# Optimization experiments

Measured on AMD Instinct MI355X. Metric: run time of the kernel, lower is better.

## Reference

```python
import jax, jax.numpy as jnp
import numpy as np

NUM_GROUPS = 32
EPS = 1e-5


def group_norm(x, scale, bias):
    # x: [B, C, L], normalize per (group, batch) over (C//G, L)
    B, C, L = x.shape
    G = NUM_GROUPS
    xg = x.reshape(B, G, C // G, L)
    mean = xg.mean(axis=(2, 3), keepdims=True)
    var = xg.var(axis=(2, 3), keepdims=True)
    xg = (xg - mean) * jax.lax.rsqrt(var + EPS)
    h = xg.reshape(B, C, L)
    return h * scale[None, :, None] + bias[None, :, None]


def setup_inputs() -> dict:
    key = jax.random.key(0)
    ks = jax.random.split(key, 8)
    B, C, L = 8, 512, 2048
    s = 1.0 / np.sqrt(C)
    return {
        "x": jax.random.normal(ks[0], (B, C, L), jnp.float32),
        "gn_scale": jnp.ones((C,), jnp.float32),
        "gn_bias": jnp.zeros((C,), jnp.float32),
        "wq": jax.random.normal(ks[1], (C, C), jnp.float32) * s,
        "bq": jnp.zeros((C,), jnp.float32),
        "wk": jax.random.normal(ks[2], (C, C), jnp.float32) * s,
        "bk": jnp.zeros((C,), jnp.float32),
        "wv": jax.random.normal(ks[3], (C, C), jnp.float32) * s,
        "bv": jnp.zeros((C,), jnp.float32),
        "wo": jax.random.normal(ks[4], (C, C), jnp.float32) * s,
        "bo": jnp.zeros((C,), jnp.float32),
    }


def reference(x, gn_scale, gn_bias, wq, bq, wk, bk, wv, bv, wo, bo):
    B, C, L = x.shape
    h = group_norm(x, gn_scale, gn_bias)  # [B, C, L]
    # 1x1 conv == per-position linear; produce [B, L, C] directly
    q = jnp.einsum('oc,bcl->blo', wq, h) + bq
    k = jnp.einsum('oc,bcl->blo', wk, h) + bk
    v = jnp.einsum('oc,bcl->blo', wv, h) + bv
    scale = jnp.asarray(C, x.dtype) ** -0.5
    w = jnp.einsum('bqc,bkc->bqk', q, k) * scale  # [B, L, L]
    w = jax.nn.softmax(w, axis=-1)
    a = jnp.einsum('bqk,bkc->bqc', w, v)  # [B, L, C]
    out = jnp.einsum('oc,blc->bol', wo, a) + bo[None, :, None]  # [B, C, L]
    return x + out
```

## Files before the change

kernel.cpp:

```cpp
#include <hip/hip_runtime.h>

typedef __attribute__((ext_vector_type(8))) _Float16 half8;
typedef __attribute__((ext_vector_type(4))) float floatx4;

#define AS1 __attribute__((address_space(1)))
#define AS3 __attribute__((address_space(3)))

__device__ __forceinline__ void async_load16(const void* g, void* l) {
  __builtin_amdgcn_global_load_lds((AS1 void*)(unsigned long long)g,
                                   (AS3 void*)(unsigned long long)l, 16, 0, 0);
}

__global__ __launch_bounds__(256) void gn_stats(const float* __restrict__ x,
                                                float* __restrict__ stats) {
  const int bg = blockIdx.x;
  const float4* p4 = (const float4*)(x + (long long)bg * 32768);
  const int t = threadIdx.x;
  float s = 0.f, ss = 0.f;
  for (int i = t; i < 8192; i += 256) {
    float4 v = p4[i];
    s += v.x + v.y + v.z + v.w;
    ss += v.x * v.x + v.y * v.y + v.z * v.z + v.w * v.w;
  }
#pragma unroll
  for (int off = 32; off; off >>= 1) { s += __shfl_down(s, off); ss += __shfl_down(ss, off); }
  __shared__ float rs[4], rss[4];
  if ((t & 63) == 0) { rs[t >> 6] = s; rss[t >> 6] = ss; }
  __syncthreads();
  if (t == 0) {
    s = rs[0] + rs[1] + rs[2] + rs[3];
    ss = rss[0] + rss[1] + rss[2] + rss[3];
    float mean = s * (1.f / 32768.f);
    float var = ss * (1.f / 32768.f) - mean * mean;
    stats[bg] = mean;
    stats[256 + bg] = rsqrtf(var + 1e-5f);
  }
}

__global__ __launch_bounds__(256) void gn_apply(const float* __restrict__ x,
                                                const float* __restrict__ stats,
                                                const float* __restrict__ gsc,
                                                const float* __restrict__ gbi,
                                                _Float16* __restrict__ ht) {
  __shared__ float tile[64][65];
  const int b = blockIdx.z, c0 = blockIdx.y * 64, l0 = blockIdx.x * 64;
  const int t = threadIdx.x, tr = t >> 6, tc = t & 63;
  const float* xb = x + ((long long)b * 512 + c0) * 2048 + l0;
#pragma unroll
  for (int p = 0; p < 16; ++p) {
    int row = tr + p * 4;
    tile[row][tc] = xb[(long long)row * 2048 + tc];
  }
  __syncthreads();
  const int c = c0 + tc;
  const int bg = b * 32 + (c >> 4);
  const float mean = stats[bg], rstd = stats[256 + bg];
  const float sc = gsc[c] * rstd;
  const float off = gbi[c] - mean * sc;
  _Float16* hb = ht + ((long long)b * 2048 + l0) * 512 + c0;
#pragma unroll
  for (int p = 0; p < 16; ++p) {
    int l = tr + p * 4;
    hb[(long long)l * 512 + tc] = (_Float16)(tile[tc][l] * sc + off);
  }
}

__global__ __launch_bounds__(256) void cast_w(const float* __restrict__ w0, const float* __restrict__ w1,
                                              const float* __restrict__ w2, const float* __restrict__ w3,
                                              const float* __restrict__ bq, const float* __restrict__ bk,
                                              _Float16* __restrict__ outw, float* __restrict__ bqk) {
  const long long i = (long long)blockIdx.x * 256 + threadIdx.x;
  if (blockIdx.x < 4096) {
    const int m = (int)(i >> 18);
    const int r = (int)(i & 262143);
    const float* w = (m == 0) ? w0 : (m == 1) ? w1 : (m == 2) ? w2 : w3;
    outw[i] = (_Float16)w[r];
  } else {
    const int j = (int)(i - 4096LL * 256);
    bqk[j] = (j < 512) ? bq[j] : bk[j - 512];
  }
}

template <int BIAS_MODE , int OUT_TYPE , bool RESIDUAL>
__global__ __launch_bounds__(256) void gemm_bt(
    const _Float16* __restrict__ A, long long sA, int lda,
    const _Float16* __restrict__ Bt, long long sB, int ldb,
    void* __restrict__ Cv, long long sC, int ldc,
    const float* __restrict__ bias,
    const float* __restrict__ resid, long long sR,
    float alpha, int K) {
  __shared__ __align__(16) _Float16 lsa[128 * 64];
  __shared__ __align__(16) _Float16 lsb[128 * 64];
  const int tid = threadIdx.x;
  const int wave = tid >> 6, lane = tid & 63;
  const int bz = blockIdx.x;
  const int m0 = blockIdx.y * 128, n0 = blockIdx.z * 128;
  A += (long long)bz * sA;
  Bt += (long long)bz * sB;

  const bool isA = (wave < 2);
  const _Float16* gsrc = isA ? A : Bt;
  const int ld = isA ? lda : ldb;
  const int rbase = (wave & 1) * 64;
  const int t0 = isA ? m0 : n0;
  _Float16* lbase = (isA ? lsa : lsb) + rbase * 64;
  const int grow = t0 + rbase + (lane >> 3);
  const int gcol = ((lane & 7) ^ ((lane >> 3) & 7)) * 8;

  floatx4 acc[4][4] = {};
  const int mw = (wave >> 1) * 64, nw = (wave & 1) * 64;
  const int fm = lane & 15;
  const int quad = lane >> 4;

  for (int k0 = 0; k0 < K; k0 += 64) {
    __syncthreads();
    const _Float16* g = gsrc + (long long)grow * ld + k0 + gcol;
#pragma unroll
    for (int s = 0; s < 8; ++s)
      async_load16(g + (long long)s * 8 * ld, lbase + s * 512);
    __syncthreads();
#pragma unroll
    for (int kk = 0; kk < 2; ++kk) {
      const int ca = quad + 4 * kk;
      const int cs = (ca ^ (fm & 7)) * 8;
      half8 af[4], bfr[4];
#pragma unroll
      for (int i = 0; i < 4; ++i) af[i] = *(const half8*)&lsa[(mw + 16 * i + fm) * 64 + cs];
#pragma unroll
      for (int j = 0; j < 4; ++j) bfr[j] = *(const half8*)&lsb[(nw + 16 * j + fm) * 64 + cs];
#pragma unroll
      for (int i = 0; i < 4; ++i)
#pragma unroll
        for (int j = 0; j < 4; ++j)
          acc[i][j] = __builtin_amdgcn_mfma_f32_16x16x32_f16(af[i], bfr[j], acc[i][j], 0, 0, 0);
    }
  }

  const int r0 = m0 + mw + quad * 4;
  const int c0 = n0 + nw + fm;
#pragma unroll
  for (int i = 0; i < 4; ++i) {
#pragma unroll
    for (int j = 0; j < 4; ++j) {
      const int cc = c0 + 16 * j;
#pragma unroll
      for (int t = 0; t < 4; ++t) {
        const int rr = r0 + 16 * i + t;
        float v = acc[i][j][t] * alpha;
        if (BIAS_MODE == 1) v += bias[cc];
        if (BIAS_MODE == 2) v += bias[rr];
        if (RESIDUAL) v += resid[(long long)bz * sR + (long long)rr * ldc + cc];
        const long long off = (long long)bz * sC + (long long)rr * ldc + cc;
        if (OUT_TYPE == 0) ((float*)Cv)[off] = v;
        else ((_Float16*)Cv)[off] = (_Float16)v;
      }
    }
  }
}

__global__ __launch_bounds__(256) void softmax_inplace(_Float16* __restrict__ S) {
  const long long row = (long long)blockIdx.y * 2048 + blockIdx.x;
  _Float16* p = S + row * 2048;
  const int t = threadIdx.x;
  union U { float4 f; _Float16 h[8]; } u;
  u.f = ((const float4*)p)[t];
  float v[8];
  float mx = -3e38f;
#pragma unroll
  for (int i = 0; i < 8; ++i) { v[i] = (float)u.h[i]; mx = fmaxf(mx, v[i]); }
#pragma unroll
  for (int off = 32; off; off >>= 1) mx = fmaxf(mx, __shfl_down(mx, off));
  __shared__ float red[4];
  if ((t & 63) == 0) red[t >> 6] = mx;
  __syncthreads();
  mx = fmaxf(fmaxf(red[0], red[1]), fmaxf(red[2], red[3]));
  float s = 0.f;
#pragma unroll
  for (int i = 0; i < 8; ++i) { v[i] = __expf(v[i] - mx); s += v[i]; }
#pragma unroll
  for (int off = 32; off; off >>= 1) s += __shfl_down(s, off);
  __syncthreads();
  if ((t & 63) == 0) red[t >> 6] = s;
  __syncthreads();
  s = red[0] + red[1] + red[2] + red[3];
  const float inv = 1.f / s;
#pragma unroll
  for (int i = 0; i < 8; ++i) u.h[i] = (_Float16)(v[i] * inv);
  ((float4*)p)[t] = u.f;
}

extern "C" void kernel_launch(void* const* d_in, const int* in_sizes, int n_in,
                              void* d_out, int out_size, void* d_ws, size_t ws_size,
                              hipStream_t stream) {
  const float* x = (const float*)d_in[0];
  const float* gsc = (const float*)d_in[1];
  const float* gbi = (const float*)d_in[2];
  const float* wq = (const float*)d_in[3];
  const float* bq = (const float*)d_in[4];
  const float* wk = (const float*)d_in[5];
  const float* bk = (const float*)d_in[6];
  const float* wv = (const float*)d_in[7];
  const float* bv = (const float*)d_in[8];
  const float* wo = (const float*)d_in[9];
  const float* bo = (const float*)d_in[10];
  float* out = (float*)d_out;

  char* ws = (char*)d_ws;
  float* stats = (float*)ws;
  float* bqk = (float*)(ws + 2048);
  _Float16* wbf = (_Float16*)(ws + 8192);
  _Float16* ht = wbf + 4 * 262144;
  const long long EB = 8LL * 2048 * 512;
  _Float16* qk = ht + EB;
  _Float16* vm = qk + 2 * EB;
  _Float16* Sb = vm + EB;
  _Float16* at = ht;

  gn_stats<<<256, 256, 0, stream>>>(x, stats);
  gn_apply<<<dim3(32, 8, 8), 256, 0, stream>>>(x, stats, gsc, gbi, ht);
  cast_w<<<4100, 256, 0, stream>>>(wq, wk, wv, wo, bq, bk, wbf, bqk);

  const float scale = 0.044194173824159216f;
  gemm_bt<1, 1, false><<<dim3(8, 16, 8), 256, 0, stream>>>(
      ht, 1048576LL, 512, wbf, 0LL, 512, qk, 2097152LL, 1024, bqk, nullptr, 0LL, 1.f, 512);
  gemm_bt<2, 1, false><<<dim3(8, 4, 16), 256, 0, stream>>>(
      wbf + 2 * 262144, 0LL, 512, ht, 1048576LL, 512, vm, 1048576LL, 2048, bv, nullptr, 0LL, 1.f, 512);
  gemm_bt<0, 1, false><<<dim3(8, 16, 16), 256, 0, stream>>>(
      qk, 2097152LL, 1024, qk + 512, 2097152LL, 1024, Sb, 4194304LL, 2048, nullptr, nullptr, 0LL, scale, 512);
  softmax_inplace<<<dim3(2048, 8), 256, 0, stream>>>(Sb);
  gemm_bt<0, 1, false><<<dim3(8, 16, 4), 256, 0, stream>>>(
      Sb, 4194304LL, 2048, vm, 1048576LL, 2048, at, 1048576LL, 512, nullptr, nullptr, 0LL, 1.f, 2048);
  gemm_bt<2, 0, true><<<dim3(8, 4, 16), 256, 0, stream>>>(
      wbf + 3 * 262144, 0LL, 512, at, 1048576LL, 512, out, 1048576LL, 2048, bo, x, 1048576LL, 1.f, 512);
}
```

Measured before the change: 301.9 us.

## Fuse QK^T, softmax and PV into a single flash-attention kernel

Removes the separate score GEMM, in-place softmax and PV GEMM, and replaces them with one kernel. It keeps the Q fragments in registers, streams 32-key K/V tiles through double-buffered LDS with async global-to-LDS loads, and applies an online softmax with running max and sum. This avoids writing and re-reading the 8x2048x2048 fp16 score matrix and cuts two launches. In exchange it runs at one wave per SIMD with very high register use, and each block re-reads the whole K/V for its batch, which adds L2 pressure.

Measured after the change: 393.9 us. 30.5% more time.

```diff
diff --git a/kernel.cpp b/kernel.cpp
--- a/kernel.cpp
+++ b/kernel.cpp
@@ -158,35 +158,135 @@
   }
 }
 
-__global__ __launch_bounds__(256) void softmax_inplace(_Float16* __restrict__ S) {
-  const long long row = (long long)blockIdx.y * 2048 + blockIdx.x;
-  _Float16* p = S + row * 2048;
-  const int t = threadIdx.x;
-  union U { float4 f; _Float16 h[8]; } u;
-  u.f = ((const float4*)p)[t];
-  float v[8];
-  float mx = -3e38f;
-#pragma unroll
-  for (int i = 0; i < 8; ++i) { v[i] = (float)u.h[i]; mx = fmaxf(mx, v[i]); }
-#pragma unroll
-  for (int off = 32; off; off >>= 1) mx = fmaxf(mx, __shfl_down(mx, off));
-  __shared__ float red[4];
-  if ((t & 63) == 0) red[t >> 6] = mx;
+__global__ __launch_bounds__(256, 1) void flash_attn(
+    const _Float16* __restrict__ qk,
+    const _Float16* __restrict__ vm,
+    _Float16* __restrict__ at) {
+  __shared__ __align__(16) _Float16 kbuf[2][32 * 512];
+  __shared__ __align__(16) _Float16 vbuf[2][512 * 32];
+  __shared__ __align__(16) _Float16 Pls[4][16 * 40];
+  const int tid = threadIdx.x, wave = tid >> 6, lane = tid & 63;
+  const int fm = lane & 15, quad = lane >> 4;
+  const int b = blockIdx.x, q0 = blockIdx.y * 64;
+  const _Float16* qb = qk + (long long)b * 2097152;
+  const _Float16* kb = qb + 512;
+  const _Float16* vb = vm + (long long)b * 1048576;
+
+  half8 qf[16];
+  {
+    const _Float16* qrow = qb + (long long)(q0 + 16 * wave + fm) * 1024 + quad * 8;
+#pragma unroll
+    for (int ks = 0; ks < 16; ++ks) {
+      half8 h = *(const half8*)(qrow + ks * 32);
+#pragma unroll
+      for (int e = 0; e < 8; ++e) h[e] = (_Float16)((float)h[e] * 0.044194173824159216f);
+      qf[ks] = h;
+    }
+  }
+
+  floatx4 o[32] = {};
+  float m_i[4], l_i[4];
+#pragma unroll
+  for (int t = 0; t < 4; ++t) { m_i[t] = -1e30f; l_i[t] = 0.f; }
+
+#pragma unroll
+  for (int s = 0; s < 8; ++s) {
+    int i = s * 256 + tid;
+    int row = i >> 6, ch = i & 63;
+    async_load16(kb + (long long)row * 1024 + ((ch ^ (row & 7)) << 3), &kbuf[0][i * 8]);
+  }
+#pragma unroll
+  for (int s = 0; s < 8; ++s) {
+    int i = s * 256 + tid;
+    int row = i >> 2, ch = i & 3;
+    async_load16(vb + (long long)row * 2048 + ((ch ^ (row & 3)) << 3), &vbuf[0][i * 8]);
+  }
   __syncthreads();
-  mx = fmaxf(fmaxf(red[0], red[1]), fmaxf(red[2], red[3]));
-  float s = 0.f;
-#pragma unroll
-  for (int i = 0; i < 8; ++i) { v[i] = __expf(v[i] - mx); s += v[i]; }
-#pragma unroll
-  for (int off = 32; off; off >>= 1) s += __shfl_down(s, off);
-  __syncthreads();
-  if ((t & 63) == 0) red[t >> 6] = s;
-  __syncthreads();
-  s = red[0] + red[1] + red[2] + red[3];
-  const float inv = 1.f / s;
-#pragma unroll
-  for (int i = 0; i < 8; ++i) u.h[i] = (_Float16)(v[i] * inv);
-  ((float4*)p)[t] = u.f;
+
+  for (int kt = 0; kt < 64; ++kt) {
+    const int cur = kt & 1;
+    if (kt < 63) {
+      const int l0 = (kt + 1) * 32;
+      const int nxt = cur ^ 1;
+#pragma unroll
+      for (int s = 0; s < 8; ++s) {
+        int i = s * 256 + tid;
+        int row = i >> 6, ch = i & 63;
+        async_load16(kb + (long long)(l0 + row) * 1024 + ((ch ^ (row & 7)) << 3),
+                     &kbuf[nxt][i * 8]);
+      }
+#pragma unroll
+      for (int s = 0; s < 8; ++s) {
+        int i = s * 256 + tid;
+        int row = i >> 2, ch = i & 3;
+        async_load16(vb + (long long)row * 2048 + l0 + ((ch ^ (row & 3)) << 3),
+                     &vbuf[nxt][i * 8]);
+      }
+    }
+
+    floatx4 sacc[2] = {};
+#pragma unroll
+    for (int ks = 0; ks < 16; ++ks) {
+#pragma unroll
+      for (int j = 0; j < 2; ++j) {
+        const int ch = (ks * 4 + quad) ^ (fm & 7);
+        half8 bf = *(const half8*)&kbuf[cur][(16 * j + fm) * 512 + ch * 8];
+        sacc[j] = __builtin_amdgcn_mfma_f32_16x16x32_f16(qf[ks], bf, sacc[j], 0, 0, 0);
+      }
+    }
+
+    float alpha[4];
+#pragma unroll
+    for (int t = 0; t < 4; ++t) {
+      float mx = fmaxf(sacc[0][t], sacc[1][t]);
+#pragma unroll
+      for (int d = 1; d < 16; d <<= 1) mx = fmaxf(mx, __shfl_xor(mx, d));
+      float mn = fmaxf(m_i[t], mx);
+      alpha[t] = __expf(m_i[t] - mn);
+      m_i[t] = mn;
+      float rs = 0.f;
+#pragma unroll
+      for (int j = 0; j < 2; ++j) {
+        float p = __expf(sacc[j][t] - mn);
+        sacc[j][t] = p;
+        rs += p;
+      }
+#pragma unroll
+      for (int d = 1; d < 16; d <<= 1) rs += __shfl_xor(rs, d);
+      l_i[t] = l_i[t] * alpha[t] + rs;
+    }
+
+#pragma unroll
+    for (int j = 0; j < 2; ++j)
+#pragma unroll
+      for (int t = 0; t < 4; ++t)
+        Pls[wave][(quad * 4 + t) * 40 + 16 * j + fm] = (_Float16)sacc[j][t];
+
+#pragma unroll
+    for (int j = 0; j < 32; ++j) {
+      o[j][0] *= alpha[0]; o[j][1] *= alpha[1];
+      o[j][2] *= alpha[2]; o[j][3] *= alpha[3];
+    }
+
+    half8 pf = *(const half8*)&Pls[wave][fm * 40 + quad * 8];
+#pragma unroll
+    for (int j = 0; j < 32; ++j) {
+      const int ch = quad ^ (fm & 3);
+      half8 vf = *(const half8*)&vbuf[cur][(16 * j + fm) * 32 + ch * 8];
+      o[j] = __builtin_amdgcn_mfma_f32_16x16x32_f16(pf, vf, o[j], 0, 0, 0);
+    }
+    __syncthreads();
+  }
+
+  float inv[4];
+#pragma unroll
+  for (int t = 0; t < 4; ++t) inv[t] = 1.f / l_i[t];
+  _Float16* ob = at + ((long long)b * 2048 + q0 + 16 * wave) * 512;
+#pragma unroll
+  for (int j = 0; j < 32; ++j)
+#pragma unroll
+    for (int t = 0; t < 4; ++t)
+      ob[(quad * 4 + t) * 512 + 16 * j + fm] = (_Float16)(o[j][t] * inv[t]);
 }
 
 extern "C" void kernel_launch(void* const* d_in, const int* in_sizes, int n_in,
@@ -211,25 +311,19 @@
   _Float16* wbf = (_Float16*)(ws + 8192);
   _Float16* ht = wbf + 4 * 262144;
   const long long EB = 8LL * 2048 * 512;
-  _Float16* qk = ht + EB;
-  _Float16* vm = qk + 2 * EB;
-  _Float16* Sb = vm + EB;
+  _Float16* qkb = ht + EB;
+  _Float16* vm = qkb + 2 * EB;
   _Float16* at = ht;
 
   gn_stats<<<256, 256, 0, stream>>>(x, stats);
   gn_apply<<<dim3(32, 8, 8), 256, 0, stream>>>(x, stats, gsc, gbi, ht);
   cast_w<<<4100, 256, 0, stream>>>(wq, wk, wv, wo, bq, bk, wbf, bqk);
 
-  const float scale = 0.044194173824159216f;
   gemm_bt<1, 1, false><<<dim3(8, 16, 8), 256, 0, stream>>>(
-      ht, 1048576LL, 512, wbf, 0LL, 512, qk, 2097152LL, 1024, bqk, nullptr, 0LL, 1.f, 512);
+      ht, 1048576LL, 512, wbf, 0LL, 512, qkb, 2097152LL, 1024, bqk, nullptr, 0LL, 1.f, 512);
   gemm_bt<2, 1, false><<<dim3(8, 4, 16), 256, 0, stream>>>(
       wbf + 2 * 262144, 0LL, 512, ht, 1048576LL, 512, vm, 1048576LL, 2048, bv, nullptr, 0LL, 1.f, 512);
-  gemm_bt<0, 1, false><<<dim3(8, 16, 16), 256, 0, stream>>>(
-      qk, 2097152LL, 1024, qk + 512, 2097152LL, 1024, Sb, 4194304LL, 2048, nullptr, nullptr, 0LL, scale, 512);
-  softmax_inplace<<<dim3(2048, 8), 256, 0, stream>>>(Sb);
-  gemm_bt<0, 1, false><<<dim3(8, 16, 4), 256, 0, stream>>>(
-      Sb, 4194304LL, 2048, vm, 1048576LL, 2048, at, 1048576LL, 512, nullptr, nullptr, 0LL, 1.f, 2048);
+  flash_attn<<<dim3(8, 32), 256, 0, stream>>>(qkb, vm, at);
   gemm_bt<2, 0, true><<<dim3(8, 4, 16), 256, 0, stream>>>(
       wbf + 3 * 262144, 0LL, 512, at, 1048576LL, 512, out, 1048576LL, 2048, bo, x, 1048576LL, 1.f, 512);
 }
```
